# Kernel tuning notes

Measured on AMD Instinct MI355X. Metric: run time of the kernel, lower is better.

Reference implementation:

```python
import jax, jax.numpy as jnp
import numpy as np

K = 10  # value-iteration steps


def _conv(x, w):
    # NCHW x OIHW -> NCHW, stride 1, SAME padding (pad=2 for 5x5, pad=0 for 1x1)
    return jax.lax.conv_general_dilated(
        x, w, window_strides=(1, 1), padding='SAME',
        dimension_numbers=('NCHW', 'OIHW', 'NCHW'))


def setup_inputs() -> dict:
    key = jax.random.key(0)
    ks = jax.random.split(key, 6)
    B, H, W = 64, 64, 64
    dim_h, n_hat, n_act = 150, 8, 4
    maze = jax.random.randint(ks[0], (B, H, W), 0, 3)
    # fixed embedding table from the torch module
    emb = jnp.array([[0.0, 0.0], [1.0, 0.0], [0.0, 10.0]], dtype=jnp.float32)
    encode_w = jax.random.normal(ks[1], (dim_h, 2, 5, 5), dtype=jnp.float32) * 0.05
    encode_b = jnp.zeros((dim_h,), dtype=jnp.float32)
    r_w = jax.random.normal(ks[2], (1, dim_h, 1, 1), dtype=jnp.float32) * 0.05
    q_w = jax.random.normal(ks[3], (n_hat, 1, 5, 5), dtype=jnp.float32) * 0.05
    # torch inits self.w to zeros; use small randn so the recurrence is non-trivial
    w = jax.random.normal(ks[4], (n_hat, 1, 5, 5), dtype=jnp.float32) * 0.05
    fc_w = jax.random.normal(ks[5], (n_act, n_hat), dtype=jnp.float32) * 0.1
    return dict(maze=maze, emb=emb, encode_w=encode_w, encode_b=encode_b,
                r_w=r_w, q_w=q_w, w=w, fc_w=fc_w)


def reference(maze, emb, encode_w, encode_b, r_w, q_w, w, fc_w):
    # embed: [B,H,W] -> [B,H,W,2] -> [B,2,H,W]
    m = emb[maze].transpose(0, 3, 1, 2)
    h = _conv(m, encode_w) + encode_b[None, :, None, None]  # [B,150,H,W]
    r = _conv(h, r_w)                                        # [B,1,H,W]
    q = _conv(r, q_w)                                        # [B,8,H,W]
    wk = jnp.concatenate([q_w, w], axis=1)                   # [8,2,5,5]

    def step(q, _):
        v = jnp.max(q, axis=1, keepdims=True)                # [B,1,H,W]
        q = _conv(jnp.concatenate([r, v], axis=1), wk)       # [B,8,H,W]
        return q, None

    q, _ = jax.lax.scan(step, q, None, length=K)
    q = q.transpose(0, 2, 3, 1)                              # [B,H,W,8]
    return q @ fc_w.T                                        # [B,H,W,4]
```

## Files before the change

### kernel.cpp

```cpp
#include <hip/hip_runtime.h>
#include <hip/hip_bf16.h>


#define NHAT 8
#define DIMH 150

typedef float v2f __attribute__((ext_vector_type(2)));

__global__ __launch_bounds__(128) void prep_kernel(
    const float* __restrict__ emb, const float* __restrict__ encode_w,
    const float* __restrict__ encode_b, const float* __restrict__ r_w,
    float* __restrict__ T, float* __restrict__ beff) {
  __shared__ float weff[2][25];
  int tid = threadIdx.x;
  if (tid < 50) {
    int i = tid / 25, k = tid % 25;
    float s = 0.f;
    for (int c = 0; c < DIMH; ++c)
      s += r_w[c] * encode_w[c * 50 + i * 25 + k];
    weff[i][k] = s;
  }
  if (tid == 64) {
    float s = 0.f;
    for (int c = 0; c < DIMH; ++c) s += r_w[c] * encode_b[c];
    *beff = s;
  }
  __syncthreads();
  if (tid < 100) {
    int val = tid / 25, k = tid % 25;
    float t = 0.f;
    if (val < 3) t = weff[0][k] * emb[val * 2] + weff[1][k] * emb[val * 2 + 1];
    T[val * 25 + k] = t;
  }
}

__global__ __launch_bounds__(256) void rq_kernel(
    const int* __restrict__ maze, const float* __restrict__ Tg,
    const float* __restrict__ beffg, const float* __restrict__ q_w,
    float* __restrict__ q0g) {
  __shared__ float Ts[4][25];
  __shared__ float bsh;
  __shared__ v2f qw2[25][4];
  __shared__ unsigned char mzt[24][68];
  __shared__ float rt[20][68];

  int tid = threadIdx.x;
  int b = blockIdx.y, A0 = blockIdx.x * 16;

  if (tid < 100) Ts[tid / 25][tid % 25] = Tg[tid];
  if (tid == 100) bsh = *beffg;
  if (tid >= 128 && tid < 228) {
    int t2 = tid - 128;
    int k = t2 >> 2, j = t2 & 3;
    qw2[k][j] = (v2f){q_w[(2 * j) * 25 + k], q_w[(2 * j + 1) * 25 + k]};
  }
  for (int i = tid; i < 24 * 68; i += 256) {
    int mr = i / 68, mc = i % 68;
    int gy = A0 - 4 + mr, gx = mc - 2;
    unsigned char v = 3;
    if (gy >= 0 && gy < 64 && gx >= 0 && gx < 64)
      v = (unsigned char)maze[(b * 64 + gy) * 64 + gx];
    mzt[mr][mc] = v;
  }
  __syncthreads();
  for (int i = tid; i < 20 * 68; i += 256) {
    int rr = i / 68, cc = i % 68;
    int gy = A0 - 2 + rr, gx = cc - 2;
    float v = 0.f;
    if (gy >= 0 && gy < 64 && gx >= 0 && gx < 64) {
      v = bsh;
#pragma unroll
      for (int ky = 0; ky < 5; ++ky)
#pragma unroll
        for (int kx = 0; kx < 5; ++kx)
          v += Ts[mzt[rr + ky][cc - 2 + kx]][ky * 5 + kx];
    }
    rt[rr][cc] = v;
  }
  __syncthreads();
  for (int i = tid; i < 16 * 64; i += 256) {
    int ly = i >> 6, gx = i & 63;
    int gy = A0 + ly;
    v2f acc[4];
#pragma unroll
    for (int j = 0; j < 4; ++j) acc[j] = (v2f){0.f, 0.f};
#pragma unroll
    for (int ky = 0; ky < 5; ++ky)
#pragma unroll
      for (int kx = 0; kx < 5; ++kx) {
        int k = ky * 5 + kx;
        float vv = rt[ly + ky][gx + kx];
        v2f vv2 = (v2f){vv, vv};
#pragma unroll
        for (int j = 0; j < 4; ++j) acc[j] += qw2[k][j] * vv2;
      }
    float* dst = q0g + ((size_t)(b * 4096 + gy * 64 + gx)) * NHAT;
    ((float4*)dst)[0] = make_float4(acc[0].x, acc[0].y, acc[1].x, acc[1].y);
    ((float4*)dst)[1] = make_float4(acc[2].x, acc[2].y, acc[3].x, acc[3].y);
  }
}

__global__ __launch_bounds__(512, 1) void vi_kernel(
    const float* __restrict__ q0g, const float* __restrict__ w,
    const float* __restrict__ fc_w, float* __restrict__ out) {
  __shared__ float vbuf[2][64][68];
  __shared__ v2f wl2[25][4];
  __shared__ float fcs[4][NHAT];

  int tid = threadIdx.x;
  int b = blockIdx.y, a0 = blockIdx.x * 16;
  int wave = tid >> 6, gx = tid & 63;

  if (tid < 100) {
    int k = tid >> 2, j = tid & 3;
    wl2[k][j] = (v2f){w[(2 * j) * 25 + k], w[(2 * j + 1) * 25 + k]};
  } else if (tid >= 128 && tid < 160) {
    int t = tid - 128;
    fcs[t >> 3][t & 7] = fc_w[t];
  }
  for (int i = tid; i < 2 * 64 * 68; i += 512) ((float*)vbuf)[i] = 0.f;
  __syncthreads();

  v2f wr[4][25];
#pragma unroll
  for (int k = 0; k < 25; ++k) {
#pragma unroll
    for (int j = 0; j < 4; ++j) wr[j][k] = wl2[k][j];
  }

  const float* q0b = q0g + (size_t)b * 4096 * NHAT;
  int cur = 0;

  {
    int s = max(0, a0 - 20), e = min(64, a0 + 36);
    for (int r = s + wave; r < e; r += 8) {
      const float4* p = (const float4*)(q0b + ((size_t)r * 64 + gx) * NHAT);
      float4 f0 = p[0], f1 = p[1];
      float m = fmaxf(fmaxf(fmaxf(f0.x, f0.y), fmaxf(f0.z, f0.w)),
                      fmaxf(fmaxf(f1.x, f1.y), fmaxf(f1.z, f1.w)));
      vbuf[0][r - a0 + 22][gx + 2] = m;
    }
  }
  __syncthreads();

  for (int t = 1; t <= 10; ++t) {
    int hh = 2 * (10 - t);
    int s = max(0, a0 - hh), e = min(64, a0 + 16 + hh);
    for (int r = s + wave; r < e; r += 8) {
      int lr = r - a0 + 22;
      const float4* p = (const float4*)(q0b + ((size_t)r * 64 + gx) * NHAT);
      float4 f0 = p[0], f1 = p[1];
      v2f a0v = (v2f){0.f, 0.f}, a1v = (v2f){0.f, 0.f};
      v2f a2v = (v2f){0.f, 0.f}, a3v = (v2f){0.f, 0.f};
#pragma unroll
      for (int ky = 0; ky < 5; ++ky) {
        const float* row = &vbuf[cur][lr - 2 + ky][gx];
#pragma unroll
        for (int kx = 0; kx < 5; ++kx) {
          int k = ky * 5 + kx;
          float vv = row[kx];
          v2f vv2 = (v2f){vv, vv};
          a0v += wr[0][k] * vv2;
          a1v += wr[1][k] * vv2;
          a2v += wr[2][k] * vv2;
          a3v += wr[3][k] * vv2;
        }
      }
      a0v += (v2f){f0.x, f0.y};
      a1v += (v2f){f0.z, f0.w};
      a2v += (v2f){f1.x, f1.y};
      a3v += (v2f){f1.z, f1.w};
      if (t < 10) {
        float m = fmaxf(fmaxf(fmaxf(a0v.x, a0v.y), fmaxf(a1v.x, a1v.y)),
                        fmaxf(fmaxf(a2v.x, a2v.y), fmaxf(a3v.x, a3v.y)));
        vbuf[cur ^ 1][lr][gx + 2] = m;
      } else {
        float4 o;
        float* op = &o.x;
#pragma unroll
        for (int a = 0; a < 4; ++a) {
          op[a] = fcs[a][0] * a0v.x + fcs[a][1] * a0v.y + fcs[a][2] * a1v.x +
                  fcs[a][3] * a1v.y + fcs[a][4] * a2v.x + fcs[a][5] * a2v.y +
                  fcs[a][6] * a3v.x + fcs[a][7] * a3v.y;
        }
        *(float4*)&out[((size_t)((b * 64 + r) * 64 + gx)) * 4] = o;
      }
    }
    cur ^= 1;
    if (t < 10) __syncthreads();
  }
}

extern "C" void kernel_launch(void* const* d_in, const int* in_sizes, int n_in,
                              void* d_out, int out_size, void* d_ws, size_t ws_size,
                              hipStream_t stream) {
  const int* maze = (const int*)d_in[0];
  const float* emb = (const float*)d_in[1];
  const float* encode_w = (const float*)d_in[2];
  const float* encode_b = (const float*)d_in[3];
  const float* r_w = (const float*)d_in[4];
  const float* q_w = (const float*)d_in[5];
  const float* w = (const float*)d_in[6];
  const float* fc_w = (const float*)d_in[7];
  float* out = (float*)d_out;

  float* wsf = (float*)d_ws;
  float* T = wsf;
  float* beff = wsf + 100;
  float* q0 = wsf + 128;

  prep_kernel<<<1, 128, 0, stream>>>(emb, encode_w, encode_b, r_w, T, beff);
  rq_kernel<<<dim3(4, 64), 256, 0, stream>>>(maze, T, beff, q_w, q0);
  vi_kernel<<<dim3(4, 64), 512, 0, stream>>>(q0, w, fc_w, out);
}
```

Measured before the change: 128.3 us.

## Split hat channels across wave pairs in VI kernel and widen rq blocks

New measurement: 123.7 us. -3.6%, faster.

```diff
diff --git a/kernel.cpp b/kernel.cpp
--- a/kernel.cpp
+++ b/kernel.cpp
@@ -34,7 +34,7 @@
   }
 }
 
-__global__ __launch_bounds__(256) void rq_kernel(
+__global__ __launch_bounds__(512) void rq_kernel(
     const int* __restrict__ maze, const float* __restrict__ Tg,
     const float* __restrict__ beffg, const float* __restrict__ q_w,
     float* __restrict__ q0g) {
@@ -54,7 +54,7 @@
     int k = t2 >> 2, j = t2 & 3;
     qw2[k][j] = (v2f){q_w[(2 * j) * 25 + k], q_w[(2 * j + 1) * 25 + k]};
   }
-  for (int i = tid; i < 24 * 68; i += 256) {
+  for (int i = tid; i < 24 * 68; i += 512) {
     int mr = i / 68, mc = i % 68;
     int gy = A0 - 4 + mr, gx = mc - 2;
     unsigned char v = 3;
@@ -63,7 +63,7 @@
     mzt[mr][mc] = v;
   }
   __syncthreads();
-  for (int i = tid; i < 20 * 68; i += 256) {
+  for (int i = tid; i < 20 * 68; i += 512) {
     int rr = i / 68, cc = i % 68;
     int gy = A0 - 2 + rr, gx = cc - 2;
     float v = 0.f;
@@ -78,7 +78,7 @@
     rt[rr][cc] = v;
   }
   __syncthreads();
-  for (int i = tid; i < 16 * 64; i += 256) {
+  for (int i = tid; i < 16 * 64; i += 512) {
     int ly = i >> 6, gx = i & 63;
     int gy = A0 + ly;
     v2f acc[4];
@@ -100,32 +100,30 @@
   }
 }
 
-__global__ __launch_bounds__(512, 1) void vi_kernel(
+__global__ __launch_bounds__(512, 2) void vi_kernel(
     const float* __restrict__ q0g, const float* __restrict__ w,
     const float* __restrict__ fc_w, float* __restrict__ out) {
-  __shared__ float vbuf[2][64][68];
+  __shared__ float vbuf[2][60][68];
+  __shared__ __align__(16) float tmp[52][2][64];
   __shared__ v2f wl2[25][4];
-  __shared__ float fcs[4][NHAT];
 
   int tid = threadIdx.x;
   int b = blockIdx.y, a0 = blockIdx.x * 16;
   int wave = tid >> 6, gx = tid & 63;
+  int half = wave & 1, slot = wave >> 1;
 
   if (tid < 100) {
     int k = tid >> 2, j = tid & 3;
     wl2[k][j] = (v2f){w[(2 * j) * 25 + k], w[(2 * j + 1) * 25 + k]};
-  } else if (tid >= 128 && tid < 160) {
-    int t = tid - 128;
-    fcs[t >> 3][t & 7] = fc_w[t];
-  }
-  for (int i = tid; i < 2 * 64 * 68; i += 512) ((float*)vbuf)[i] = 0.f;
-  __syncthreads();
-
-  v2f wr[4][25];
+  }
+  for (int i = tid; i < 2 * 60 * 68; i += 512) ((float*)vbuf)[i] = 0.f;
+  __syncthreads();
+
+  v2f wr0[25], wr1[25];
 #pragma unroll
   for (int k = 0; k < 25; ++k) {
-#pragma unroll
-    for (int j = 0; j < 4; ++j) wr[j][k] = wl2[k][j];
+    wr0[k] = wl2[k][2 * half];
+    wr1[k] = wl2[k][2 * half + 1];
   }
 
   const float* q0b = q0g + (size_t)b * 4096 * NHAT;
@@ -143,51 +141,84 @@
   }
   __syncthreads();
 
-  for (int t = 1; t <= 10; ++t) {
+  for (int t = 1; t <= 9; ++t) {
     int hh = 2 * (10 - t);
     int s = max(0, a0 - hh), e = min(64, a0 + 16 + hh);
-    for (int r = s + wave; r < e; r += 8) {
+    for (int r = s + slot; r < e; r += 4) {
       int lr = r - a0 + 22;
-      const float4* p = (const float4*)(q0b + ((size_t)r * 64 + gx) * NHAT);
-      float4 f0 = p[0], f1 = p[1];
-      v2f a0v = (v2f){0.f, 0.f}, a1v = (v2f){0.f, 0.f};
-      v2f a2v = (v2f){0.f, 0.f}, a3v = (v2f){0.f, 0.f};
+      const float4* p =
+          (const float4*)(q0b + ((size_t)r * 64 + gx) * NHAT + half * 4);
+      float4 q4 = *p;
+      v2f acc0 = (v2f){0.f, 0.f}, acc1 = (v2f){0.f, 0.f};
 #pragma unroll
       for (int ky = 0; ky < 5; ++ky) {
         const float* row = &vbuf[cur][lr - 2 + ky][gx];
 #pragma unroll
         for (int kx = 0; kx < 5; ++kx) {
-          int k = ky * 5 + kx;
           float vv = row[kx];
           v2f vv2 = (v2f){vv, vv};
-          a0v += wr[0][k] * vv2;
-          a1v += wr[1][k] * vv2;
-          a2v += wr[2][k] * vv2;
-          a3v += wr[3][k] * vv2;
+          acc0 += wr0[ky * 5 + kx] * vv2;
+          acc1 += wr1[ky * 5 + kx] * vv2;
         }
       }
-      a0v += (v2f){f0.x, f0.y};
-      a1v += (v2f){f0.z, f0.w};
-      a2v += (v2f){f1.x, f1.y};
-      a3v += (v2f){f1.z, f1.w};
-      if (t < 10) {
-        float m = fmaxf(fmaxf(fmaxf(a0v.x, a0v.y), fmaxf(a1v.x, a1v.y)),
-                        fmaxf(fmaxf(a2v.x, a2v.y), fmaxf(a3v.x, a3v.y)));
-        vbuf[cur ^ 1][lr][gx + 2] = m;
-      } else {
-        float4 o;
-        float* op = &o.x;
-#pragma unroll
-        for (int a = 0; a < 4; ++a) {
-          op[a] = fcs[a][0] * a0v.x + fcs[a][1] * a0v.y + fcs[a][2] * a1v.x +
-                  fcs[a][3] * a1v.y + fcs[a][4] * a2v.x + fcs[a][5] * a2v.y +
-                  fcs[a][6] * a3v.x + fcs[a][7] * a3v.y;
-        }
-        *(float4*)&out[((size_t)((b * 64 + r) * 64 + gx)) * 4] = o;
+      acc0 += (v2f){q4.x, q4.y};
+      acc1 += (v2f){q4.z, q4.w};
+      float m = fmaxf(fmaxf(acc0.x, acc0.y), fmaxf(acc1.x, acc1.y));
+      tmp[lr - 4][half][gx] = m;
+    }
+    __syncthreads();
+    int n = e - s;
+    for (int idx = tid; idx < n * 64; idx += 512) {
+      int rr = idx >> 6, px = idx & 63;
+      int lr2 = s - a0 + 22 + rr;
+      float m = fmaxf(tmp[lr2 - 4][0][px], tmp[lr2 - 4][1][px]);
+      vbuf[cur ^ 1][lr2][px + 2] = m;
+    }
+    __syncthreads();
+    cur ^= 1;
+  }
+
+  float fcp[4][4];
+#pragma unroll
+  for (int a = 0; a < 4; ++a)
+#pragma unroll
+    for (int cc = 0; cc < 4; ++cc) fcp[a][cc] = fc_w[a * 8 + 4 * half + cc];
+  float* projtmp = (float*)tmp;
+
+#pragma unroll
+  for (int i = 0; i < 4; ++i) {
+    int r = a0 + slot + 4 * i;
+    int lr = r - a0 + 22;
+    const float4* p =
+        (const float4*)(q0b + ((size_t)r * 64 + gx) * NHAT + half * 4);
+    float4 q4 = *p;
+    v2f acc0 = (v2f){0.f, 0.f}, acc1 = (v2f){0.f, 0.f};
+#pragma unroll
+    for (int ky = 0; ky < 5; ++ky) {
+      const float* row = &vbuf[cur][lr - 2 + ky][gx];
+#pragma unroll
+      for (int kx = 0; kx < 5; ++kx) {
+        float vv = row[kx];
+        v2f vv2 = (v2f){vv, vv};
+        acc0 += wr0[ky * 5 + kx] * vv2;
+        acc1 += wr1[ky * 5 + kx] * vv2;
       }
     }
-    cur ^= 1;
-    if (t < 10) __syncthreads();
+    float q0v = acc0.x + q4.x, q1v = acc0.y + q4.y;
+    float q2v = acc1.x + q4.z, q3v = acc1.y + q4.w;
+    float4 pp;
+    pp.x = fcp[0][0] * q0v + fcp[0][1] * q1v + fcp[0][2] * q2v + fcp[0][3] * q3v;
+    pp.y = fcp[1][0] * q0v + fcp[1][1] * q1v + fcp[1][2] * q2v + fcp[1][3] * q3v;
+    pp.z = fcp[2][0] * q0v + fcp[2][1] * q1v + fcp[2][2] * q2v + fcp[2][3] * q3v;
+    pp.w = fcp[3][0] * q0v + fcp[3][1] * q1v + fcp[3][2] * q2v + fcp[3][3] * q3v;
+    if (half == 1) *(float4*)&projtmp[(slot * 64 + gx) * 4] = pp;
+    __syncthreads();
+    if (half == 0) {
+      float4 o = *(const float4*)&projtmp[(slot * 64 + gx) * 4];
+      o.x += pp.x; o.y += pp.y; o.z += pp.z; o.w += pp.w;
+      *(float4*)&out[((size_t)((b * 64 + r) * 64 + gx)) * 4] = o;
+    }
+    __syncthreads();
   }
 }
 
@@ -210,6 +241,6 @@
   float* q0 = wsf + 128;
 
   prep_kernel<<<1, 128, 0, stream>>>(emb, encode_w, encode_b, r_w, T, beff);
-  rq_kernel<<<dim3(4, 64), 256, 0, stream>>>(maze, T, beff, q_w, q0);
+  rq_kernel<<<dim3(4, 64), 512, 0, stream>>>(maze, T, beff, q_w, q0);
   vi_kernel<<<dim3(4, 64), 512, 0, stream>>>(q0, w, fc_w, out);
 }
```
